# Optimization experiments

Hardware: AMD Instinct MI355X
Metric: run time of the kernel (lower is better)

## Reference

```python
import jax, jax.numpy as jnp
import numpy as np

LN_EPS = 1e-5

def setup_inputs() -> dict:
    key = jax.random.key(0)
    ks = jax.random.split(key, 10)
    B, L, D2 = 64, 512, 16  # batch, max_len_text, 2*n_degree
    V, D, C = 8000, 256, 4  # n_word, d_model, n_category
    E = (V - 1) * V + 1      # edge-weight table size
    x = jax.random.randint(ks[0], (B, L), 0, V, dtype=jnp.int32)
    nb_x = jax.random.randint(ks[1], (B, L, D2), 0, V, dtype=jnp.int32)
    w_edge = jax.random.randint(ks[2], (B, L, D2), 0, E, dtype=jnp.int32)
    emb_weight = jax.random.normal(ks[3], (V, D), jnp.float32) * 0.02
    emb_weight = emb_weight.at[0].set(0.0)  # padding_idx=0
    w_edge_table = jax.random.normal(ks[4], (E, 1), jnp.float32) * 0.02
    w_edge_table = w_edge_table.at[0].set(0.0)
    eta_table = jax.random.normal(ks[5], (V, 1), jnp.float32) * 0.02
    eta_table = eta_table.at[0].set(0.0)
    ln_gamma = jnp.ones((D,), jnp.float32)
    ln_beta = jnp.zeros((D,), jnp.float32)
    fc_w = jax.random.normal(ks[6], (D, C), jnp.float32) * 0.02
    fc_b = jnp.zeros((C,), jnp.float32)
    return {"x": x, "nb_x": nb_x, "w_edge": w_edge,
            "emb_weight": emb_weight, "w_edge_table": w_edge_table,
            "eta_table": eta_table, "ln_gamma": ln_gamma, "ln_beta": ln_beta,
            "fc_w": fc_w, "fc_b": fc_b}

def _layernorm(h, gamma, beta):
    mu = jnp.mean(h, axis=-1, keepdims=True)
    var = jnp.mean(jnp.square(h - mu), axis=-1, keepdims=True)
    return (h - mu) * jax.lax.rsqrt(var + LN_EPS) * gamma + beta

def reference(x, nb_x, w_edge, emb_weight, w_edge_table, eta_table,
              ln_gamma, ln_beta, fc_w, fc_b):
    # idx_nodes: (B, L, 2*deg + 1) -- neighbors then self
    idx_nodes = jnp.concatenate([nb_x, x[..., None]], axis=-1)
    emb_nodes = emb_weight[idx_nodes]                  # (B, L, 2d+1, D)
    emb_nodes = _layernorm(emb_nodes, ln_gamma, ln_beta)
    we = w_edge_table[w_edge]                          # (B, L, 2d, 1)
    msg_nb = jnp.max(we * emb_nodes[:, :, :-1, :], axis=2)  # (B, L, D)
    eta = eta_table[x]                                 # (B, L, 1)
    h_node = (1.0 - eta) * msg_nb + eta * emb_nodes[:, :, -1, :]
    scores = h_node.sum(axis=1) @ fc_w + fc_b          # (B, C)
    return scores
```

## Files before the change

kernel.cpp:

```cpp
#include <hip/hip_runtime.h>
#include <math.h>

#define DV   256
#define BB   64
#define LL   512
#define DEG2 16
#define VV   8000
#define CC   4
#define LPW  4
#define NW   4
#define LCB  (LPW*NW)
#define NLC  (LL/LCB)
#define LN_EPS 1e-5f

typedef _Float16 half4 __attribute__((ext_vector_type(4)));
typedef float    f32x4 __attribute__((ext_vector_type(4)));

__global__ void __launch_bounds__(64) ln_rows_kernel(
    const float* __restrict__ emb, const float* __restrict__ gamma,
    const float* __restrict__ beta, half4* __restrict__ out)
{
    const int row = blockIdx.x;
    const int ln  = threadIdx.x;

    const f32x4 v = ((const f32x4*)(emb + row * DV))[ln];

    float s = v[0] + v[1] + v[2] + v[3];
    #pragma unroll
    for (int off = 32; off > 0; off >>= 1) s += __shfl_xor(s, off);
    const float mu = s * (1.0f / DV);

    f32x4 c;
    #pragma unroll
    for (int k = 0; k < 4; ++k) c[k] = v[k] - mu;

    float q = c[0]*c[0] + c[1]*c[1] + c[2]*c[2] + c[3]*c[3];
    #pragma unroll
    for (int off = 32; off > 0; off >>= 1) q += __shfl_xor(q, off);
    const float rs = rsqrtf(q * (1.0f / DV) + LN_EPS);

    const f32x4 g  = ((const f32x4*)gamma)[ln];
    const f32x4 bt = ((const f32x4*)beta)[ln];

    half4 h;
    #pragma unroll
    for (int k = 0; k < 4; ++k) h[k] = (_Float16)(c[k] * rs * g[k] + bt[k]);
    out[row * 64 + ln] = h;
}

__global__ void __launch_bounds__(256) gnn_kernel(
    const int*   __restrict__ nb_x,
    const int*   __restrict__ w_edge,
    const float* __restrict__ we_table,
    const int*   __restrict__ x,
    const float* __restrict__ eta_table,
    const half4* __restrict__ norm_emb,
    float*       __restrict__ h_part)
{
    const int b   = blockIdx.x;
    const int lc  = blockIdx.y;
    const int tid = threadIdx.x;
    const int w   = tid >> 6;
    const int ln  = tid & 63;

    const int l0   = lc * LCB + w * LPW;
    const int base = b * LL + l0;

    const int   nbv = __builtin_nontemporal_load(nb_x   + base * DEG2 + ln);
    const int   eiv = __builtin_nontemporal_load(w_edge + base * DEG2 + ln);
    const float wev = __builtin_nontemporal_load(we_table + eiv);

    int xv = 0; float etv = 0.0f;
    if (ln < LPW) { xv = x[base + ln]; etv = eta_table[xv]; }

    f32x4 acc = {0.0f, 0.0f, 0.0f, 0.0f};

    #pragma unroll
    for (int li = 0; li < LPW; ++li) {
        half4 m;
        m[0] = m[1] = m[2] = m[3] = (_Float16)(-65504.0f);

        #pragma unroll
        for (int j = 0; j < DEG2; ++j) {
            const int   lane = li * DEG2 + j;
            const int   idx  = __shfl(nbv, lane);
            const float wej  = __shfl(wev, lane);
            half4 wh;
            wh[0] = wh[1] = wh[2] = wh[3] = (_Float16)wej;
            const half4 e = norm_emb[idx * 64 + ln];
            m = __builtin_elementwise_max(m, wh * e);
        }

        const int   sidx = __shfl(xv, li);
        const float eta  = __shfl(etv, li);
        const half4 se   = norm_emb[sidx * 64 + ln];
        const float om   = 1.0f - eta;

        #pragma unroll
        for (int k = 0; k < 4; ++k)
            acc[k] += om * (float)m[k] + eta * (float)se[k];
    }

    __shared__ float s_acc[NW][DV];
    ((f32x4*)s_acc[w])[ln] = acc;
    __syncthreads();
    if (w == 0) {
        f32x4 r0 = ((f32x4*)s_acc[0])[ln];
        f32x4 r1 = ((f32x4*)s_acc[1])[ln];
        f32x4 r2 = ((f32x4*)s_acc[2])[ln];
        f32x4 r3 = ((f32x4*)s_acc[3])[ln];
        f32x4 r;
        #pragma unroll
        for (int k = 0; k < 4; ++k) r[k] = r0[k] + r1[k] + r2[k] + r3[k];
        __builtin_nontemporal_store(r, (f32x4*)(h_part + (b * NLC + lc) * DV) + ln);
    }
}

__global__ void __launch_bounds__(256) fc_kernel(
    const float* __restrict__ h_part,
    const float* __restrict__ fc_w,
    const float* __restrict__ fc_b,
    float*       __restrict__ out)
{
    const int b  = blockIdx.x;
    const int d  = threadIdx.x;
    const int w  = d >> 6;
    const int ln = d & 63;

    float h = 0.0f;
    #pragma unroll 8
    for (int lc = 0; lc < NLC; ++lc)
        h += h_part[(b * NLC + lc) * DV + d];

    float p[CC];
    #pragma unroll
    for (int c = 0; c < CC; ++c) p[c] = h * fc_w[d * CC + c];

    #pragma unroll
    for (int c = 0; c < CC; ++c)
        #pragma unroll
        for (int off = 32; off > 0; off >>= 1) p[c] += __shfl_xor(p[c], off);

    __shared__ float s_red[4][CC];
    if (ln == 0) {
        #pragma unroll
        for (int c = 0; c < CC; ++c) s_red[w][c] = p[c];
    }
    __syncthreads();
    if (d < CC)
        out[b * CC + d] = s_red[0][d] + s_red[1][d] + s_red[2][d] + s_red[3][d] + fc_b[d];
}

extern "C" void kernel_launch(void* const* d_in, const int* in_sizes, int n_in,
                              void* d_out, int out_size, void* d_ws, size_t ws_size,
                              hipStream_t stream) {
    const int*   x        = (const int*)  d_in[0];
    const int*   nb_x     = (const int*)  d_in[1];
    const int*   w_edge   = (const int*)  d_in[2];
    const float* emb_w    = (const float*)d_in[3];
    const float* we_table = (const float*)d_in[4];
    const float* eta_tab  = (const float*)d_in[5];
    const float* ln_gamma = (const float*)d_in[6];
    const float* ln_beta  = (const float*)d_in[7];
    const float* fc_w     = (const float*)d_in[8];
    const float* fc_b     = (const float*)d_in[9];
    float* out = (float*)d_out;

    char* ws = (char*)d_ws;
    half4* norm_emb = (half4*)(ws);
    float* h_part   = (float*)(ws + 4096000);

    ln_rows_kernel<<<VV, 64, 0, stream>>>(emb_w, ln_gamma, ln_beta, norm_emb);

    dim3 grid2(BB, NLC);
    gnn_kernel<<<grid2, 256, 0, stream>>>(nb_x, w_edge, we_table, x, eta_tab,
                                          norm_emb, h_part);

    fc_kernel<<<BB, 256, 0, stream>>>(h_part, fc_w, fc_b, out);
}
```

Measured before the change: 44.67 us.

## Split normalized embedding table into XCD-pinned feature halves and pre-gather edge weights

The normalized fp16 embedding table is stored as two 128-feature slices, and each gnn block works on only one slice. Block indices are mapped so that the four XCDs handling one slice only ever touch that 2 MB half, which is meant to keep the random row gathers inside each XCD's L2. Each wavefront now gathers two neighbor rows per load, one per 32-lane half, then combines the halves with a cross-half max. A separate kernel gathers the edge weights beforehand. The cost is doubled index and metadata loads across slices, an extra kernel launch with its own round trip through memory, and a dependence on the hardware assigning blocks to XCDs round-robin.

```diff
diff --git a/kernel.cpp b/kernel.cpp
--- a/kernel.cpp
+++ b/kernel.cpp
@@ -11,10 +11,24 @@
 #define NW   4
 #define LCB  (LPW*NW)
 #define NLC  (LL/LCB)
+#define NSL  2
+#define DSL  (DV/NSL)
 #define LN_EPS 1e-5f
 
 typedef _Float16 half4 __attribute__((ext_vector_type(4)));
 typedef float    f32x4 __attribute__((ext_vector_type(4)));
+
+__device__ __forceinline__ int rl(int v, int lane) {
+    return __builtin_amdgcn_readlane(v, lane);
+}
+__device__ __forceinline__ float rlf(float v, int lane) {
+    return __int_as_float(__builtin_amdgcn_readlane(__float_as_int(v), lane));
+}
+__device__ __forceinline__ half4 swap32(half4 v) {
+    int2 i = __builtin_bit_cast(int2, v);
+    int2 s; s.x = __shfl_xor(i.x, 32); s.y = __shfl_xor(i.y, 32);
+    return __builtin_bit_cast(half4, s);
+}
 
 __global__ void __launch_bounds__(64) ln_rows_kernel(
     const float* __restrict__ emb, const float* __restrict__ gamma,
@@ -45,74 +59,105 @@
     half4 h;
     #pragma unroll
     for (int k = 0; k < 4; ++k) h[k] = (_Float16)(c[k] * rs * g[k] + bt[k]);
-    out[row * 64 + ln] = h;
-}
-
-__global__ void __launch_bounds__(256) gnn_kernel(
+
+    const int sl = ln >> 5;
+    const int cc = ln & 31;
+    out[((size_t)sl * VV + row) * 32 + cc] = h;
+}
+
+__global__ void __launch_bounds__(256) wgather_kernel(
+    const int* __restrict__ w_edge, const float* __restrict__ we_table,
+    float* __restrict__ we_flat)
+{
+    const int i = blockIdx.x * 256 + threadIdx.x;
+    we_flat[i] = we_table[w_edge[i]];
+}
+
+__global__ void __launch_bounds__(256) gnn_slice_kernel(
     const int*   __restrict__ nb_x,
-    const int*   __restrict__ w_edge,
-    const float* __restrict__ we_table,
     const int*   __restrict__ x,
+    const float* __restrict__ we_flat,
     const float* __restrict__ eta_table,
-    const half4* __restrict__ norm_emb,
+    const half4* __restrict__ norm_emb2,
     float*       __restrict__ h_part)
 {
-    const int b   = blockIdx.x;
-    const int lc  = blockIdx.y;
+    const int blk = blockIdx.x;
+    const int xcd = blk & 7;
+    const int u   = blk >> 3;
+    const int sl  = xcd >> 2;
+    const int q   = (xcd & 3) + (u << 2);
+    const int b   = q >> 5;
+    const int lc  = q & 31;
+
     const int tid = threadIdx.x;
     const int w   = tid >> 6;
     const int ln  = tid & 63;
+    const int c   = ln & 31;
 
     const int l0   = lc * LCB + w * LPW;
     const int base = b * LL + l0;
+    const size_t sOff = (size_t)sl * VV;
 
     const int   nbv = __builtin_nontemporal_load(nb_x   + base * DEG2 + ln);
-    const int   eiv = __builtin_nontemporal_load(w_edge + base * DEG2 + ln);
-    const float wev = __builtin_nontemporal_load(we_table + eiv);
-
+    const float wev = __builtin_nontemporal_load(we_flat + base * DEG2 + ln);
     int xv = 0; float etv = 0.0f;
     if (ln < LPW) { xv = x[base + ln]; etv = eta_table[xv]; }
 
     f32x4 acc = {0.0f, 0.0f, 0.0f, 0.0f};
 
     #pragma unroll
-    for (int li = 0; li < LPW; ++li) {
-        half4 m;
-        m[0] = m[1] = m[2] = m[3] = (_Float16)(-65504.0f);
-
-        #pragma unroll
-        for (int j = 0; j < DEG2; ++j) {
-            const int   lane = li * DEG2 + j;
-            const int   idx  = __shfl(nbv, lane);
-            const float wej  = __shfl(wev, lane);
-            half4 wh;
-            wh[0] = wh[1] = wh[2] = wh[3] = (_Float16)wej;
-            const half4 e = norm_emb[idx * 64 + ln];
-            m = __builtin_elementwise_max(m, wh * e);
+    for (int t = 0; t < LPW / 2; ++t) {
+        const int sx0 = rl(xv, 2 * t);
+        const int sx1 = rl(xv, 2 * t + 1);
+        const int srow = (ln < 32) ? sx0 : sx1;
+        const half4 sp = norm_emb2[(sOff + srow) * 32 + c];
+        const half4 sw = swap32(sp);
+        const half4 se0 = (ln < 32) ? sp : sw;
+        const half4 se1 = (ln < 32) ? sw : sp;
+
+        #pragma unroll
+        for (int li2 = 0; li2 < 2; ++li2) {
+            const int li = 2 * t + li2;
+            half4 m;
+            m[0] = m[1] = m[2] = m[3] = (_Float16)(-65504.0f);
+
+            #pragma unroll
+            for (int k = 0; k < 8; ++k) {
+                const int jlo = li * DEG2 + k;
+                const int ilo = rl(nbv, jlo);
+                const int ihi = rl(nbv, jlo + 8);
+                const float wlo = rlf(wev, jlo);
+                const float whi = rlf(wev, jlo + 8);
+                const int   idx = (ln < 32) ? ilo : ihi;
+                const float wej = (ln < 32) ? wlo : whi;
+                half4 w4; w4[0] = w4[1] = w4[2] = w4[3] = (_Float16)wej;
+                const half4 e = norm_emb2[(sOff + idx) * 32 + c];
+                m = __builtin_elementwise_max(m, w4 * e);
+            }
+            m = __builtin_elementwise_max(m, swap32(m));
+
+            const float eta = rlf(etv, li);
+            const float om  = 1.0f - eta;
+            const half4 se  = li2 ? se1 : se0;
+            #pragma unroll
+            for (int k = 0; k < 4; ++k)
+                acc[k] += om * (float)m[k] + eta * (float)se[k];
         }
-
-        const int   sidx = __shfl(xv, li);
-        const float eta  = __shfl(etv, li);
-        const half4 se   = norm_emb[sidx * 64 + ln];
-        const float om   = 1.0f - eta;
-
-        #pragma unroll
-        for (int k = 0; k < 4; ++k)
-            acc[k] += om * (float)m[k] + eta * (float)se[k];
     }
 
-    __shared__ float s_acc[NW][DV];
-    ((f32x4*)s_acc[w])[ln] = acc;
+    __shared__ float s_acc[NW][DSL];
+    ((f32x4*)s_acc[w])[c] = acc;
     __syncthreads();
-    if (w == 0) {
-        f32x4 r0 = ((f32x4*)s_acc[0])[ln];
-        f32x4 r1 = ((f32x4*)s_acc[1])[ln];
-        f32x4 r2 = ((f32x4*)s_acc[2])[ln];
-        f32x4 r3 = ((f32x4*)s_acc[3])[ln];
+    if (w == 0 && ln < 32) {
+        f32x4 r0 = ((f32x4*)s_acc[0])[c];
+        f32x4 r1 = ((f32x4*)s_acc[1])[c];
+        f32x4 r2 = ((f32x4*)s_acc[2])[c];
+        f32x4 r3 = ((f32x4*)s_acc[3])[c];
         f32x4 r;
         #pragma unroll
         for (int k = 0; k < 4; ++k) r[k] = r0[k] + r1[k] + r2[k] + r3[k];
-        __builtin_nontemporal_store(r, (f32x4*)(h_part + (b * NLC + lc) * DV) + ln);
+        __builtin_nontemporal_store(r,
+            (f32x4*)(h_part + ((size_t)(b * NLC + lc)) * DV + sl * DSL) + c);
     }
 }
 
@@ -167,14 +212,16 @@
     float* out = (float*)d_out;
 
     char* ws = (char*)d_ws;
-    half4* norm_emb = (half4*)(ws);
-    float* h_part   = (float*)(ws + 4096000);
-
-    ln_rows_kernel<<<VV, 64, 0, stream>>>(emb_w, ln_gamma, ln_beta, norm_emb);
-
-    dim3 grid2(BB, NLC);
-    gnn_kernel<<<grid2, 256, 0, stream>>>(nb_x, w_edge, we_table, x, eta_tab,
-                                          norm_emb, h_part);
+    half4* norm_emb2 = (half4*)(ws);
+    float* h_part    = (float*)(ws + 4096000);
+    float* we_flat   = (float*)(ws + 4096000 + 2097152);
+
+    ln_rows_kernel<<<VV, 64, 0, stream>>>(emb_w, ln_gamma, ln_beta, norm_emb2);
+
+    wgather_kernel<<<(BB * LL * DEG2) / 256, 256, 0, stream>>>(w_edge, we_table, we_flat);
+
+    gnn_slice_kernel<<<BB * NLC * NSL, 256, 0, stream>>>(
+        nb_x, x, we_flat, eta_tab, norm_emb2, h_part);
 
     fc_kernel<<<BB, 256, 0, stream>>>(h_part, fc_w, fc_b, out);
 }
```

After: 50.60 us. 13.3% more time.

## Split wave into half-waves gathering 16-byte half8 rows, combine max across halves

Applied to the files above, without the earlier changes.

Each wave is now split into two 32-lane halves. Each lane loads 8 fp16 values (16 bytes) per gather, and each half covers 8 of the 16 neighbors, so there are 8 gather iterations per position instead of 16. The partial maxima from the two halves are combined with an xor-32 shuffle. Wider loads and half the loop count should cut instruction and latency overhead in the gather loop. Self-index and eta are now broadcast with readlane instead of shuffle. The cost is an extra cross-lane swap per position, and half the lanes sit idle during the shared-memory store.

```diff
diff --git a/kernel.cpp b/kernel.cpp
--- a/kernel.cpp
+++ b/kernel.cpp
@@ -9,12 +9,27 @@
 #define CC   4
 #define LPW  4
 #define NW   4
-#define LCB  (LPW*NW)
-#define NLC  (LL/LCB)
+#define NLC  32
 #define LN_EPS 1e-5f
 
 typedef _Float16 half4 __attribute__((ext_vector_type(4)));
+typedef _Float16 half8 __attribute__((ext_vector_type(8)));
 typedef float    f32x4 __attribute__((ext_vector_type(4)));
+typedef int      i32x4 __attribute__((ext_vector_type(4)));
+
+__device__ __forceinline__ int rl(int v, int lane) {
+    return __builtin_amdgcn_readlane(v, lane);
+}
+__device__ __forceinline__ float rlf(float v, int lane) {
+    return __int_as_float(__builtin_amdgcn_readlane(__float_as_int(v), lane));
+}
+__device__ __forceinline__ half8 swap32h8(half8 v) {
+    i32x4 i = __builtin_bit_cast(i32x4, v);
+    i32x4 s;
+    #pragma unroll
+    for (int k = 0; k < 4; ++k) s[k] = __shfl_xor(i[k], 32);
+    return __builtin_bit_cast(half8, s);
+}
 
 __global__ void __launch_bounds__(64) ln_rows_kernel(
     const float* __restrict__ emb, const float* __restrict__ gamma,
@@ -54,7 +69,7 @@
     const float* __restrict__ we_table,
     const int*   __restrict__ x,
     const float* __restrict__ eta_table,
-    const half4* __restrict__ norm_emb,
+    const half8* __restrict__ norm_emb,
     float*       __restrict__ h_part)
 {
     const int b   = blockIdx.x;
@@ -62,8 +77,10 @@
     const int tid = threadIdx.x;
     const int w   = tid >> 6;
     const int ln  = tid & 63;
-
-    const int l0   = lc * LCB + w * LPW;
+    const int c   = ln & 31;
+    const int hi8 = (ln >> 5) << 3;
+
+    const int l0   = lc * 16 + w * LPW;
     const int base = b * LL + l0;
 
     const int   nbv = __builtin_nontemporal_load(nb_x   + base * DEG2 + ln);
@@ -73,36 +90,43 @@
     int xv = 0; float etv = 0.0f;
     if (ln < LPW) { xv = x[base + ln]; etv = eta_table[xv]; }
 
-    f32x4 acc = {0.0f, 0.0f, 0.0f, 0.0f};
+    float acc[8] = {0,0,0,0,0,0,0,0};
 
     #pragma unroll
     for (int li = 0; li < LPW; ++li) {
-        half4 m;
-        m[0] = m[1] = m[2] = m[3] = (_Float16)(-65504.0f);
-
-        #pragma unroll
-        for (int j = 0; j < DEG2; ++j) {
-            const int   lane = li * DEG2 + j;
-            const int   idx  = __shfl(nbv, lane);
-            const float wej  = __shfl(wev, lane);
-            half4 wh;
-            wh[0] = wh[1] = wh[2] = wh[3] = (_Float16)wej;
-            const half4 e = norm_emb[idx * 64 + ln];
-            m = __builtin_elementwise_max(m, wh * e);
+        half8 m;
+        #pragma unroll
+        for (int k = 0; k < 8; ++k) m[k] = (_Float16)(-65504.0f);
+
+        #pragma unroll
+        for (int k = 0; k < 8; ++k) {
+            const int   jsrc = li * DEG2 + k + hi8;
+            const int   idx  = __shfl(nbv, jsrc);
+            const float wj   = __shfl(wev, jsrc);
+            half8 w8;
+            #pragma unroll
+            for (int q = 0; q < 8; ++q) w8[q] = (_Float16)wj;
+            const half8 e = norm_emb[idx * 32 + c];
+            m = __builtin_elementwise_max(m, w8 * e);
         }
-
-        const int   sidx = __shfl(xv, li);
-        const float eta  = __shfl(etv, li);
-        const half4 se   = norm_emb[sidx * 64 + ln];
+        m = __builtin_elementwise_max(m, swap32h8(m));
+
+        const int   sidx = rl(xv, li);
+        const float eta  = rlf(etv, li);
+        const half8 se   = norm_emb[sidx * 32 + c];
         const float om   = 1.0f - eta;
-
-        #pragma unroll
-        for (int k = 0; k < 4; ++k)
+        #pragma unroll
+        for (int k = 0; k < 8; ++k)
             acc[k] += om * (float)m[k] + eta * (float)se[k];
     }
 
     __shared__ float s_acc[NW][DV];
-    ((f32x4*)s_acc[w])[ln] = acc;
+    if (ln < 32) {
+        f32x4 a0 = {acc[0], acc[1], acc[2], acc[3]};
+        f32x4 a1 = {acc[4], acc[5], acc[6], acc[7]};
+        ((f32x4*)&s_acc[w][c * 8])[0] = a0;
+        ((f32x4*)&s_acc[w][c * 8])[1] = a1;
+    }
     __syncthreads();
     if (w == 0) {
         f32x4 r0 = ((f32x4*)s_acc[0])[ln];
@@ -112,7 +136,7 @@
         f32x4 r;
         #pragma unroll
         for (int k = 0; k < 4; ++k) r[k] = r0[k] + r1[k] + r2[k] + r3[k];
-        __builtin_nontemporal_store(r, (f32x4*)(h_part + (b * NLC + lc) * DV) + ln);
+        __builtin_nontemporal_store(r, (f32x4*)(h_part + (size_t)(b * NLC + lc) * DV) + ln);
     }
 }
 
@@ -130,7 +154,7 @@
     float h = 0.0f;
     #pragma unroll 8
     for (int lc = 0; lc < NLC; ++lc)
-        h += h_part[(b * NLC + lc) * DV + d];
+        h += h_part[(size_t)(b * NLC + lc) * DV + d];
 
     float p[CC];
     #pragma unroll
@@ -141,7 +165,7 @@
         #pragma unroll
         for (int off = 32; off > 0; off >>= 1) p[c] += __shfl_xor(p[c], off);
 
-    __shared__ float s_red[4][CC];
+    __shared__ float s_red[NW][CC];
     if (ln == 0) {
         #pragma unroll
         for (int c = 0; c < CC; ++c) s_red[w][c] = p[c];
@@ -174,7 +198,7 @@
 
     dim3 grid2(BB, NLC);
     gnn_kernel<<<grid2, 256, 0, stream>>>(nb_x, w_edge, we_table, x, eta_tab,
-                                          norm_emb, h_part);
+                                          (const half8*)norm_emb, h_part);
 
     fc_kernel<<<BB, 256, 0, stream>>>(h_part, fc_w, fc_b, out);
 }
```

Result: no change. 43.90 us (-1.7%).

## Pre-gather edge weights in LN kernel and drop shared-memory reduction in GNN kernel

Applied to the files above, without the earlier changes.

The random gather of edge weights from the large edge table moves into the layernorm kernel, which writes a flat per-edge weight buffer that the GNN kernel then reads contiguously. The GNN kernel becomes two independent waves per block, and each wave stores its own partial sum, so the shared-memory reduction and the block barrier go away. The cost is an extra 2 MB write and read of the flat weights, plus a partial-sum buffer four times larger that the fc kernel must sum over 128 chunks per batch instead of 32. This lengthens the serial fc reduction.

```diff
diff --git a/kernel.cpp b/kernel.cpp
--- a/kernel.cpp
+++ b/kernel.cpp
@@ -8,9 +8,8 @@
 #define VV   8000
 #define CC   4
 #define LPW  4
-#define NW   4
-#define LCB  (LPW*NW)
-#define NLC  (LL/LCB)
+#define NQ   (LL/LPW)
+#define NE   (BB*LL*DEG2)
 #define LN_EPS 1e-5f
 
 typedef _Float16 half4 __attribute__((ext_vector_type(4)));
@@ -18,10 +17,15 @@
 
 __global__ void __launch_bounds__(64) ln_rows_kernel(
     const float* __restrict__ emb, const float* __restrict__ gamma,
-    const float* __restrict__ beta, half4* __restrict__ out)
+    const float* __restrict__ beta,
+    const int* __restrict__ w_edge, const float* __restrict__ we_table,
+    half4* __restrict__ out, float* __restrict__ we_flat)
 {
     const int row = blockIdx.x;
     const int ln  = threadIdx.x;
+
+    for (int g = blockIdx.x * 64 + ln; g < NE; g += VV * 64)
+        we_flat[g] = we_table[w_edge[g]];
 
     const f32x4 v = ((const f32x4*)(emb + row * DV))[ln];
 
@@ -48,27 +52,25 @@
     out[row * 64 + ln] = h;
 }
 
-__global__ void __launch_bounds__(256) gnn_kernel(
+__global__ void __launch_bounds__(128) gnn_wave_kernel(
     const int*   __restrict__ nb_x,
-    const int*   __restrict__ w_edge,
-    const float* __restrict__ we_table,
     const int*   __restrict__ x,
+    const float* __restrict__ we_flat,
     const float* __restrict__ eta_table,
     const half4* __restrict__ norm_emb,
     float*       __restrict__ h_part)
 {
-    const int b   = blockIdx.x;
-    const int lc  = blockIdx.y;
     const int tid = threadIdx.x;
-    const int w   = tid >> 6;
     const int ln  = tid & 63;
+    const int wid = blockIdx.x * 2 + (tid >> 6);
+    const int b   = wid >> 7;
+    const int lq  = wid & 127;
 
-    const int l0   = lc * LCB + w * LPW;
+    const int l0   = lq * LPW;
     const int base = b * LL + l0;
 
-    const int   nbv = __builtin_nontemporal_load(nb_x   + base * DEG2 + ln);
-    const int   eiv = __builtin_nontemporal_load(w_edge + base * DEG2 + ln);
-    const float wev = __builtin_nontemporal_load(we_table + eiv);
+    const int   nbv = __builtin_nontemporal_load(nb_x    + base * DEG2 + ln);
+    const float wev = __builtin_nontemporal_load(we_flat + base * DEG2 + ln);
 
     int xv = 0; float etv = 0.0f;
     if (ln < LPW) { xv = x[base + ln]; etv = eta_table[xv]; }
@@ -85,35 +87,22 @@
             const int   lane = li * DEG2 + j;
             const int   idx  = __shfl(nbv, lane);
             const float wej  = __shfl(wev, lane);
-            half4 wh;
-            wh[0] = wh[1] = wh[2] = wh[3] = (_Float16)wej;
+            half4 w4; w4[0] = w4[1] = w4[2] = w4[3] = (_Float16)wej;
             const half4 e = norm_emb[idx * 64 + ln];
-            m = __builtin_elementwise_max(m, wh * e);
+            m = __builtin_elementwise_max(m, w4 * e);
         }
 
         const int   sidx = __shfl(xv, li);
         const float eta  = __shfl(etv, li);
         const half4 se   = norm_emb[sidx * 64 + ln];
         const float om   = 1.0f - eta;
-
         #pragma unroll
         for (int k = 0; k < 4; ++k)
             acc[k] += om * (float)m[k] + eta * (float)se[k];
     }
 
-    __shared__ float s_acc[NW][DV];
-    ((f32x4*)s_acc[w])[ln] = acc;
-    __syncthreads();
-    if (w == 0) {
-        f32x4 r0 = ((f32x4*)s_acc[0])[ln];
-        f32x4 r1 = ((f32x4*)s_acc[1])[ln];
-        f32x4 r2 = ((f32x4*)s_acc[2])[ln];
-        f32x4 r3 = ((f32x4*)s_acc[3])[ln];
-        f32x4 r;
-        #pragma unroll
-        for (int k = 0; k < 4; ++k) r[k] = r0[k] + r1[k] + r2[k] + r3[k];
-        __builtin_nontemporal_store(r, (f32x4*)(h_part + (b * NLC + lc) * DV) + ln);
-    }
+    __builtin_nontemporal_store(acc,
+        (f32x4*)(h_part + (size_t)(b * NQ + lq) * DV) + ln);
 }
 
 __global__ void __launch_bounds__(256) fc_kernel(
@@ -129,8 +118,8 @@
 
     float h = 0.0f;
     #pragma unroll 8
-    for (int lc = 0; lc < NLC; ++lc)
-        h += h_part[(b * NLC + lc) * DV + d];
+    for (int lq = 0; lq < NQ; ++lq)
+        h += h_part[(size_t)(b * NQ + lq) * DV + d];
 
     float p[CC];
     #pragma unroll
@@ -168,13 +157,14 @@
 
     char* ws = (char*)d_ws;
     half4* norm_emb = (half4*)(ws);
-    float* h_part   = (float*)(ws + 4096000);
+    float* we_flat  = (float*)(ws + 4096000);
+    float* h_part   = (float*)(ws + 4096000 + 2097152);
 
-    ln_rows_kernel<<<VV, 64, 0, stream>>>(emb_w, ln_gamma, ln_beta, norm_emb);
+    ln_rows_kernel<<<VV, 64, 0, stream>>>(emb_w, ln_gamma, ln_beta,
+                                          w_edge, we_table, norm_emb, we_flat);
 
-    dim3 grid2(BB, NLC);
-    gnn_kernel<<<grid2, 256, 0, stream>>>(nb_x, w_edge, we_table, x, eta_tab,
-                                          norm_emb, h_part);
+    gnn_wave_kernel<<<BB * NQ / 2, 128, 0, stream>>>(
+        nb_x, x, we_flat, eta_tab, norm_emb, h_part);
 
     fc_kernel<<<BB, 256, 0, stream>>>(h_part, fc_w, fc_b, out);
 }
```

After: 49.54 us. +10.9%, slower.
